# Performance work log

Measured on AMD Instinct MI355X. Metric: run time of the kernel, lower is better.

## Reference

```python
import jax, jax.numpy as jnp
import numpy as np

BSZ, SEQ, EMBED = 2, 4096, 1024
NUM_HEADS = 16
HEAD_DIM = EMBED // NUM_HEADS
WINDOW = 256  # attention_window[layer_id]


def setup_inputs() -> dict:
    key = jax.random.key(0)
    ks = jax.random.split(key, 7)
    s = 1.0 / np.sqrt(EMBED)
    return {
        "hidden_states": jax.random.normal(ks[0], (BSZ, SEQ, EMBED), jnp.float32),
        "Wq": jax.random.normal(ks[1], (EMBED, EMBED), jnp.float32) * s,
        "bq": jnp.zeros((EMBED,), jnp.float32),
        "Wk": jax.random.normal(ks[2], (EMBED, EMBED), jnp.float32) * s,
        "bk": jnp.zeros((EMBED,), jnp.float32),
        "Wv": jax.random.normal(ks[3], (EMBED, EMBED), jnp.float32) * s,
        "bv": jnp.zeros((EMBED,), jnp.float32),
    }


def _blocks3(x, nb, w):
    # x: [b, s + 2w, h, d] -> [b, nb, 3w, h, d]; block c sees key blocks c-1, c, c+1
    b = x.shape[0]
    xb = x.reshape(b, nb + 2, w, NUM_HEADS, HEAD_DIM)
    return jnp.concatenate([xb[:, i:i + nb] for i in range(3)], axis=2)


def reference(hidden_states, Wq, bq, Wk, bk, Wv, bv):
    b, s, e = hidden_states.shape
    w = WINDOW
    nb = s // w
    q = (hidden_states @ Wq + bq) * (1.0 / np.sqrt(HEAD_DIM))
    k = hidden_states @ Wk + bk
    v = hidden_states @ Wv + bv
    q = q.reshape(b, nb, w, NUM_HEADS, HEAD_DIM)
    k = k.reshape(b, s, NUM_HEADS, HEAD_DIM)
    v = v.reshape(b, s, NUM_HEADS, HEAD_DIM)
    pad = ((0, 0), (w, w), (0, 0), (0, 0))
    kb = _blocks3(jnp.pad(k, pad), nb, w)  # [b, nb, 3w, h, d]
    vb = _blocks3(jnp.pad(v, pad), nb, w)
    # banded scores: query x in block n attends keys at global pos n*w - w + y
    scores = jnp.einsum('bnxhd,bnyhd->bnhxy', q, kb)  # [b, nb, h, w, 3w]
    x_idx = jnp.arange(w)
    y_idx = jnp.arange(3 * w)
    band = jnp.abs(y_idx[None, :] - x_idx[:, None] - w) <= w  # [w, 3w]
    kpos = jnp.arange(nb)[:, None] * w - w + y_idx[None, :]   # [nb, 3w]
    inb = (kpos >= 0) & (kpos < s)
    mask = band[None, :, :] & inb[:, None, :]                 # [nb, w, 3w]
    scores = jnp.where(mask[None, :, None, :, :], scores, -jnp.inf)
    probs = jax.nn.softmax(scores.astype(jnp.float32), axis=-1).astype(v.dtype)
    attn = jnp.einsum('bnhxy,bnyhd->bnxhd', probs, vb)        # [b, nb, w, h, d]
    return attn.reshape(b, s, e)
```

## Files before the change

### kernel.cpp

```cpp
#include <hip/hip_runtime.h>
#include <stdint.h>

#define SEQ    4096
#define EMBED  1024
#define NHEAD  16
#define HDIM   64
#define WIN    256
#define BSZ    2
#define M_TOT  (BSZ * SEQ)
#define N_QKV  3072
#define N_QK   2048
#define K_DIM  1024
#define LOG2E  1.4426950408889634f

typedef __attribute__((ext_vector_type(8))) __bf16 bf16x8;
typedef __attribute__((ext_vector_type(4))) float  f32x4;

__device__ __forceinline__ unsigned short f2bf(float f) {
  union { float f; unsigned int u; } c; c.f = f;
  unsigned int u = c.u;
  unsigned int r = (u + 0x7FFFu + ((u >> 16) & 1u)) >> 16;
  return (unsigned short)r;
}

__device__ __forceinline__ unsigned int cvt_pk_bf16(float lo, float hi) {
  unsigned int r;
  asm("v_cvt_pk_bf16_f32 %0, %1, %2" : "=v"(r) : "v"(lo), "v"(hi));
  return r;
}

__device__ __forceinline__ void gl2lds16(const void* g, void* l) {
  __builtin_amdgcn_global_load_lds((const __attribute__((address_space(1))) void*)g,
                                   (__attribute__((address_space(3))) void*)l, 16, 0, 0);
}

__global__ __launch_bounds__(256) void cvt_h(const float* __restrict__ in,
                                             unsigned short* __restrict__ out) {
  int i = (blockIdx.x * 256 + threadIdx.x) * 4;
  float4 v = *(const float4*)(in + i);
  ushort4 o;
  o.x = f2bf(v.x); o.y = f2bf(v.y); o.z = f2bf(v.z); o.w = f2bf(v.w);
  *(ushort4*)(out + i) = o;
}

__global__ __launch_bounds__(256) void cvt_w(const float* __restrict__ Wq,
                                             const float* __restrict__ Wk,
                                             const float* __restrict__ Wv,
                                             unsigned short* __restrict__ Wt) {
  __shared__ float t[32][33];
  int z = blockIdx.z;
  const float* W = (z == 0) ? Wq : (z == 1) ? Wk : Wv;
  int kb = blockIdx.x * 32, nb = blockIdx.y * 32;
  int tx = threadIdx.x, ty = threadIdx.y;
  for (int it = 0; it < 4; ++it) {
    int k = kb + ty + it * 8;
    t[ty + it * 8][tx] = W[(size_t)k * 1024 + nb + tx];
  }
  __syncthreads();
  for (int it = 0; it < 4; ++it) {
    int n = nb + ty + it * 8;
    Wt[(size_t)(z * 1024 + n) * 1024 + kb + tx] = f2bf(t[tx][ty + it * 8]);
  }
}

__global__ __launch_bounds__(512, 2) void qkv_gemm(const unsigned short* __restrict__ A,
                                                   const unsigned short* __restrict__ Bt,
                                                   const float* __restrict__ bq,
                                                   const float* __restrict__ bk,
                                                   const float* __restrict__ bv,
                                                   unsigned short* __restrict__ C,
                                                   unsigned short* __restrict__ Vt) {
  __shared__ unsigned short As[2][256 * 64];
  __shared__ unsigned short Bs[2][256 * 64];
  int tid  = threadIdx.x;
  int lane = tid & 63, wave = tid >> 6;
  int ln   = lane & 15, quad = lane >> 4;
  int flat = blockIdx.y * 12 + blockIdx.x;
  int swz  = (flat & 7) * 48 + (flat >> 3);
  int m0 = (swz / 12) * 256, n0 = (swz % 12) * 256;
  int wy = wave >> 2, wx = wave & 3;
  f32x4 acc[8][4];
  for (int i = 0; i < 8; ++i)
    for (int j = 0; j < 4; ++j) acc[i][j] = (f32x4){0.f, 0.f, 0.f, 0.f};

#define STAGE(buf, k0)                                                          \
  do {                                                                          \
    for (int sweep = 0; sweep < 4; ++sweep) {                                   \
      int chunk = sweep * 512 + tid;                               \
      int row = chunk >> 3, c = chunk & 7;                                      \
      int cg = c ^ (row & 7);                                                   \
      gl2lds16(A + (size_t)(m0 + row) * K_DIM + (k0) + cg * 8,                  \
               &As[buf][chunk * 8]);                                            \
    }                                                                           \
    for (int sweep = 0; sweep < 4; ++sweep) {                                   \
      int chunk = sweep * 512 + tid;                                            \
      int row = chunk >> 3, c = chunk & 7;                                      \
      int cg = c ^ (row & 7);                                                   \
      gl2lds16(Bt + (size_t)(n0 + row) * K_DIM + (k0) + cg * 8,                 \
               &Bs[buf][chunk * 8]);                                            \
    }                                                                           \
  } while (0)

  STAGE(0, 0);
  __syncthreads();

  for (int t = 0; t < 16; ++t) {
    int cur = t & 1;
    if (t < 15) { STAGE(cur ^ 1, (t + 1) * 64); }
    const unsigned short* as = As[cur];
    const unsigned short* bs = Bs[cur];
    for (int ks2 = 0; ks2 < 2; ++ks2) {
      bf16x8 af[8], bfr[4];
      for (int i = 0; i < 8; ++i) {
        int row = wy * 128 + i * 16 + ln;
        int c = (ks2 * 4 + quad) ^ (row & 7);
        af[i] = *(const bf16x8*)&as[row * 64 + c * 8];
      }
      for (int j = 0; j < 4; ++j) {
        int row = wx * 64 + j * 16 + ln;
        int c = (ks2 * 4 + quad) ^ (row & 7);
        bfr[j] = *(const bf16x8*)&bs[row * 64 + c * 8];
      }
      __builtin_amdgcn_s_setprio(1);
      for (int i = 0; i < 8; ++i)
        for (int j = 0; j < 4; ++j)
          acc[i][j] = __builtin_amdgcn_mfma_f32_16x16x32_bf16(af[i], bfr[j], acc[i][j], 0, 0, 0);
      __builtin_amdgcn_s_setprio(0);
    }
    __syncthreads();
  }
#undef STAGE

  if (n0 < N_QK) {
    for (int j = 0; j < 4; ++j) {
      int n = n0 + wx * 64 + j * 16 + ln;
      float bias, scl;
      if (n < 1024) { bias = bq[n];        scl = 0.125f * LOG2E; }
      else          { bias = bk[n - 1024]; scl = 1.f; }
      for (int i = 0; i < 8; ++i) {
        int mb = m0 + wy * 128 + i * 16 + quad * 4;
        for (int r = 0; r < 4; ++r) {
          float v = (acc[i][j][r] + bias) * scl;
          C[(size_t)(mb + r) * N_QK + n] = f2bf(v);
        }
      }
    }
  } else {
    for (int j = 0; j < 4; ++j) {
      int n  = n0 + wx * 64 + j * 16 + ln;
      int hd = n - 2048;
      float bias = bv[hd];
      for (int i = 0; i < 8; ++i) {
        int mb  = m0 + wy * 128 + i * 16 + quad * 4;
        int bb  = mb >> 12;
        int pos = mb & (SEQ - 1);
        ushort4 pk;
        pk.x = f2bf(acc[i][j][0] + bias);
        pk.y = f2bf(acc[i][j][1] + bias);
        pk.z = f2bf(acc[i][j][2] + bias);
        pk.w = f2bf(acc[i][j][3] + bias);
        *(ushort4*)&Vt[((size_t)bb * (NHEAD * HDIM) + hd) * SEQ + pos] = pk;
      }
    }
  }
}

__global__ __launch_bounds__(256) void attn(const unsigned short* __restrict__ qk,
                                            const unsigned short* __restrict__ vtg,
                                            float* __restrict__ out) {
  __shared__ unsigned short Kl[64 * 72];
  __shared__ unsigned short Vl[64 * 72];
  int tid  = threadIdx.x;
  int lane = tid & 63, wave = tid >> 6;
  int ln   = lane & 15, quad = lane >> 4;
  int bx = blockIdx.x;
  int lx = ((bx & 7) << 3) | (bx >> 3);
  int q0 = lx * 64, head = blockIdx.y, b = blockIdx.z;
  size_t baseRow = (size_t)b * SEQ;
  const unsigned short* kptr = qk + 1024;
  const unsigned short* vrow = vtg + ((size_t)(b * NHEAD + head) * HDIM) * SEQ;

  int sy = tid >> 3, sc = tid & 7;
  const unsigned short* kbase = kptr + (baseRow + sy) * (size_t)N_QK + head * HDIM + sc * 8;
  const unsigned short* vbase = vrow + (size_t)sy * SEQ + sc * 8;

  bf16x8 qf[2];
  {
    size_t ro = (baseRow + q0 + wave * 16 + ln) * (size_t)N_QK + head * HDIM + quad * 8;
    qf[0] = *(const bf16x8*)&qk[ro];
    qf[1] = *(const bf16x8*)&qk[ro + 32];
  }

  float l_st = 0.f;
  f32x4 o_acc[4];
  for (int dt = 0; dt < 4; ++dt) o_acc[dt] = (f32x4){0.f, 0.f, 0.f, 0.f};

  int lo = (q0 >= 256) ? 0 : (256 - q0) / 64;
  int hi = (SEQ + 256 - q0) / 64; if (hi > 9) hi = 9;

  uint4 pk0, pk1, pv0, pv1;
#define PREFETCH(KT)                                                        \
  {                                                                         \
    pk0 = *(const uint4*)&kbase[(size_t)(KT) * N_QK];                       \
    pk1 = *(const uint4*)&kbase[(size_t)((KT) + 32) * N_QK];                \
    pv0 = *(const uint4*)&vbase[(KT)];                                      \
    pv1 = *(const uint4*)&vbase[(size_t)32 * SEQ + (KT)];                   \
  }

  PREFETCH(q0 - 256 + lo * 64);

  int srcA = ((lane & 16) << 1) | ln;
  int srcB = srcA + 16;
  bool hiQ = (lane & 32) != 0;

  for (int t = lo; t < hi; ++t) {
    int kt = q0 - 256 + t * 64;
    __syncthreads();
    *(uint4*)&Kl[sy * 72 + sc * 8]        = pk0;
    *(uint4*)&Kl[(sy + 32) * 72 + sc * 8] = pk1;
    *(uint4*)&Vl[sy * 72 + sc * 8]        = pv0;
    *(uint4*)&Vl[(sy + 32) * 72 + sc * 8] = pv1;
    __syncthreads();

    if (t + 1 < hi) { PREFETCH(kt + 64); }

    f32x4 s[4];
    __builtin_amdgcn_s_setprio(1);
    for (int nt = 0; nt < 4; ++nt) {
      bf16x8 kf0 = *(const bf16x8*)&Kl[(nt * 16 + ln) * 72 + quad * 8];
      bf16x8 kf1 = *(const bf16x8*)&Kl[(nt * 16 + ln) * 72 + 32 + quad * 8];
      f32x4 z = (f32x4){0.f, 0.f, 0.f, 0.f};
      z = __builtin_amdgcn_mfma_f32_16x16x32_bf16(kf0, qf[0], z, 0, 0, 0);
      z = __builtin_amdgcn_mfma_f32_16x16x32_bf16(kf1, qf[1], z, 0, 0, 0);
      s[nt] = z;
    }
    __builtin_amdgcn_s_setprio(0);

    if (t == 0 || t == 8) {
      int qq = q0 + wave * 16 + ln;
      for (int nt = 0; nt < 4; ++nt) {
        int kb = kt + nt * 16 + quad * 4 - qq;
        for (int r = 0; r < 4; ++r) {
          int dd = kb + r;
          if (dd < -WIN || dd > WIN) s[nt][r] = -INFINITY;
        }
      }
    }

    float rs = 0.f;
    for (int nt = 0; nt < 4; ++nt)
      for (int r = 0; r < 4; ++r) {
        float p = exp2f(s[nt][r]);
        s[nt][r] = p;
        rs += p;
      }
    l_st += rs;

    unsigned int p01[4], p23[4];
    for (int nt = 0; nt < 4; ++nt) {
      p01[nt] = cvt_pk_bf16(s[nt][0], s[nt][1]);
      p23[nt] = cvt_pk_bf16(s[nt][2], s[nt][3]);
    }

    for (int ks = 0; ks < 2; ++ks) {
      int ntA = 2 * ks, ntB = 2 * ks + 1;
      unsigned int a0 = (unsigned int)__shfl((int)p01[ntA], srcA);
      unsigned int a1 = (unsigned int)__shfl((int)p23[ntA], srcA);
      unsigned int a2 = (unsigned int)__shfl((int)p01[ntA], srcB);
      unsigned int a3 = (unsigned int)__shfl((int)p23[ntA], srcB);
      unsigned int b0 = (unsigned int)__shfl((int)p01[ntB], srcA);
      unsigned int b1 = (unsigned int)__shfl((int)p23[ntB], srcA);
      unsigned int b2 = (unsigned int)__shfl((int)p01[ntB], srcB);
      unsigned int b3 = (unsigned int)__shfl((int)p23[ntB], srcB);
      union { uint4 u; bf16x8 v; } pf;
      pf.u.x = hiQ ? b0 : a0;
      pf.u.y = hiQ ? b1 : a1;
      pf.u.z = hiQ ? b2 : a2;
      pf.u.w = hiQ ? b3 : a3;
      __builtin_amdgcn_s_setprio(1);
      for (int dt = 0; dt < 4; ++dt) {
        bf16x8 vf = *(const bf16x8*)&Vl[(dt * 16 + ln) * 72 + ks * 32 + quad * 8];
        o_acc[dt] = __builtin_amdgcn_mfma_f32_16x16x32_bf16(vf, pf.v, o_acc[dt], 0, 0, 0);
      }
      __builtin_amdgcn_s_setprio(0);
    }
  }

  float l = l_st;
  l += __shfl_xor(l, 16);
  l += __shfl_xor(l, 32);
  float inv = 1.0f / l;
  int qpos = q0 + wave * 16 + ln;
  float* ob = out + (baseRow + qpos) * (size_t)EMBED + head * HDIM + quad * 4;
  for (int dt = 0; dt < 4; ++dt) {
    float4 v;
    v.x = o_acc[dt][0] * inv;
    v.y = o_acc[dt][1] * inv;
    v.z = o_acc[dt][2] * inv;
    v.w = o_acc[dt][3] * inv;
    *(float4*)(ob + dt * 16) = v;
  }
#undef PREFETCH
}

extern "C" void kernel_launch(void* const* d_in, const int* in_sizes, int n_in,
                              void* d_out, int out_size, void* d_ws, size_t ws_size,
                              hipStream_t stream) {
  const float* h  = (const float*)d_in[0];
  const float* Wq = (const float*)d_in[1];
  const float* bq = (const float*)d_in[2];
  const float* Wk = (const float*)d_in[3];
  const float* bk = (const float*)d_in[4];
  const float* Wv = (const float*)d_in[5];
  const float* bv = (const float*)d_in[6];
  float* out = (float*)d_out;

  unsigned short* h_bf  = (unsigned short*)d_ws;
  unsigned short* wt_bf = h_bf + (size_t)M_TOT * K_DIM;
  unsigned short* qk    = wt_bf + (size_t)N_QKV * K_DIM;
  unsigned short* vtg   = qk + (size_t)M_TOT * N_QK;

  cvt_h<<<(M_TOT * K_DIM) / 1024, 256, 0, stream>>>(h, h_bf);
  cvt_w<<<dim3(32, 32, 3), dim3(32, 8), 0, stream>>>(Wq, Wk, Wv, wt_bf);
  qkv_gemm<<<dim3(12, 32), 512, 0, stream>>>(h_bf, wt_bf, bq, bk, bv, qk, vtg);
  attn<<<dim3(SEQ / 64, NHEAD, BSZ), 256, 0, stream>>>(qk, vtg, out);
}
```

Baseline: 220.7 us.

## Split QKV GEMM tile into quadrant-staged pipeline with interleaved async loads

Restructures the QKV GEMM main loop into four quadrant MFMA phases. The next K-tile's A and B halves are issued as async global-to-LDS loads between those phases, gated by explicit vmcnt waits and raw s_barrier instead of one bulk stage followed by __syncthreads. Fragment loads are reordered so the A and B quarters are reused across phases, and the loops are fully unrolled. The aim is to hide global memory latency under the MFMA work with finer-grained overlap. The cost is more barriers per iteration and fragile hand-managed waitcnt/buffer reuse ordering.

Result: faster. 214.5 us (-2.8%).

```diff
diff --git a/kernel.cpp b/kernel.cpp
--- a/kernel.cpp
+++ b/kernel.cpp
@@ -80,65 +80,158 @@
   int m0 = (swz / 12) * 256, n0 = (swz % 12) * 256;
   int wy = wave >> 2, wx = wave & 3;
   f32x4 acc[8][4];
+#pragma unroll
   for (int i = 0; i < 8; ++i)
+#pragma unroll
     for (int j = 0; j < 4; ++j) acc[i][j] = (f32x4){0.f, 0.f, 0.f, 0.f};
 
-#define STAGE(buf, k0)                                                          \
-  do {                                                                          \
-    for (int sweep = 0; sweep < 4; ++sweep) {                                   \
-      int chunk = sweep * 512 + tid;                               \
-      int row = chunk >> 3, c = chunk & 7;                                      \
-      int cg = c ^ (row & 7);                                                   \
-      gl2lds16(A + (size_t)(m0 + row) * K_DIM + (k0) + cg * 8,                  \
-               &As[buf][chunk * 8]);                                            \
-    }                                                                           \
-    for (int sweep = 0; sweep < 4; ++sweep) {                                   \
-      int chunk = sweep * 512 + tid;                                            \
-      int row = chunk >> 3, c = chunk & 7;                                      \
-      int cg = c ^ (row & 7);                                                   \
-      gl2lds16(Bt + (size_t)(n0 + row) * K_DIM + (k0) + cg * 8,                 \
-               &Bs[buf][chunk * 8]);                                            \
-    }                                                                           \
+  int c8 = tid & 7;
+  int aR[2][2], bR[2][2];
+#pragma unroll
+  for (int s = 0; s < 2; ++s) {
+    int rir = s * 64 + (tid >> 3);
+    int la = (rir & 63) | ((rir & 64) << 1);
+    int lb = (rir & 31) | ((rir >> 5) << 6);
+    aR[0][s] = la;  aR[1][s] = la + 64;
+    bR[0][s] = lb;  bR[1][s] = lb + 32;
+  }
+
+#define STG_A(buf, half, kt)                                                     \
+  do {                                                                           \
+    _Pragma("unroll")                                                            \
+    for (int s = 0; s < 2; ++s) {                                                \
+      int lr = aR[half][s]; int cg = c8 ^ (lr & 7);                              \
+      gl2lds16(A + (size_t)(m0 + lr) * K_DIM + (kt) * 64 + cg * 8,               \
+               &As[buf][lr * 64 + c8 * 8]);                                      \
+    }                                                                            \
   } while (0)
-
-  STAGE(0, 0);
-  __syncthreads();
-
+#define STG_B(buf, half, kt)                                                     \
+  do {                                                                           \
+    _Pragma("unroll")                                                            \
+    for (int s = 0; s < 2; ++s) {                                                \
+      int lr = bR[half][s]; int cg = c8 ^ (lr & 7);                              \
+      gl2lds16(Bt + (size_t)(n0 + lr) * K_DIM + (kt) * 64 + cg * 8,              \
+               &Bs[buf][lr * 64 + c8 * 8]);                                      \
+    }                                                                            \
+  } while (0)
+
+  STG_A(0, 0, 0); STG_B(0, 0, 0); STG_B(0, 1, 0); STG_A(0, 1, 0);
+  STG_A(1, 0, 1); STG_B(1, 0, 1); STG_B(1, 1, 1);
+  asm volatile("s_waitcnt vmcnt(6)" ::: "memory");
+  __builtin_amdgcn_s_barrier();
+
+  bf16x8 af[4][2], bv0[2][2], bv1[2][2];
+  int aBase = wy * 128, bBase = wx * 64;
+
+#pragma unroll 1
   for (int t = 0; t < 16; ++t) {
     int cur = t & 1;
-    if (t < 15) { STAGE(cur ^ 1, (t + 1) * 64); }
     const unsigned short* as = As[cur];
     const unsigned short* bs = Bs[cur];
-    for (int ks2 = 0; ks2 < 2; ++ks2) {
-      bf16x8 af[8], bfr[4];
-      for (int i = 0; i < 8; ++i) {
-        int row = wy * 128 + i * 16 + ln;
-        int c = (ks2 * 4 + quad) ^ (row & 7);
-        af[i] = *(const bf16x8*)&as[row * 64 + c * 8];
-      }
-      for (int j = 0; j < 4; ++j) {
-        int row = wx * 64 + j * 16 + ln;
-        int c = (ks2 * 4 + quad) ^ (row & 7);
-        bfr[j] = *(const bf16x8*)&bs[row * 64 + c * 8];
-      }
-      __builtin_amdgcn_s_setprio(1);
-      for (int i = 0; i < 8; ++i)
-        for (int j = 0; j < 4; ++j)
-          acc[i][j] = __builtin_amdgcn_mfma_f32_16x16x32_bf16(af[i], bfr[j], acc[i][j], 0, 0, 0);
-      __builtin_amdgcn_s_setprio(0);
-    }
-    __syncthreads();
-  }
-#undef STAGE
+
+#pragma unroll
+    for (int i2 = 0; i2 < 4; ++i2) {
+      int row = aBase + i2 * 16 + ln;
+#pragma unroll
+      for (int ks = 0; ks < 2; ++ks) {
+        int c = (ks * 4 + quad) ^ (row & 7);
+        af[i2][ks] = *(const bf16x8*)&as[row * 64 + c * 8];
+      }
+    }
+#pragma unroll
+    for (int j2 = 0; j2 < 2; ++j2) {
+      int row = bBase + j2 * 16 + ln;
+#pragma unroll
+      for (int ks = 0; ks < 2; ++ks) {
+        int c = (ks * 4 + quad) ^ (row & 7);
+        bv0[j2][ks] = *(const bf16x8*)&bs[row * 64 + c * 8];
+      }
+    }
+    if (t < 15) STG_A(cur ^ 1, 1, t + 1);
+    __builtin_amdgcn_s_barrier();
+    __builtin_amdgcn_s_setprio(1);
+#pragma unroll
+    for (int ks = 0; ks < 2; ++ks)
+#pragma unroll
+      for (int i2 = 0; i2 < 4; ++i2)
+#pragma unroll
+        for (int j2 = 0; j2 < 2; ++j2)
+          acc[i2][j2] = __builtin_amdgcn_mfma_f32_16x16x32_bf16(af[i2][ks], bv0[j2][ks], acc[i2][j2], 0, 0, 0);
+    __builtin_amdgcn_s_setprio(0);
+    __builtin_amdgcn_s_barrier();
+
+#pragma unroll
+    for (int j2 = 0; j2 < 2; ++j2) {
+      int row = bBase + 32 + j2 * 16 + ln;
+#pragma unroll
+      for (int ks = 0; ks < 2; ++ks) {
+        int c = (ks * 4 + quad) ^ (row & 7);
+        bv1[j2][ks] = *(const bf16x8*)&bs[row * 64 + c * 8];
+      }
+    }
+    if (t < 14) STG_A(cur, 0, t + 2);
+    __builtin_amdgcn_s_barrier();
+    __builtin_amdgcn_s_setprio(1);
+#pragma unroll
+    for (int ks = 0; ks < 2; ++ks)
+#pragma unroll
+      for (int i2 = 0; i2 < 4; ++i2)
+#pragma unroll
+        for (int j2 = 0; j2 < 2; ++j2)
+          acc[i2][2 + j2] = __builtin_amdgcn_mfma_f32_16x16x32_bf16(af[i2][ks], bv1[j2][ks], acc[i2][2 + j2], 0, 0, 0);
+    __builtin_amdgcn_s_setprio(0);
+    __builtin_amdgcn_s_barrier();
+
+#pragma unroll
+    for (int i2 = 0; i2 < 4; ++i2) {
+      int row = aBase + 64 + i2 * 16 + ln;
+#pragma unroll
+      for (int ks = 0; ks < 2; ++ks) {
+        int c = (ks * 4 + quad) ^ (row & 7);
+        af[i2][ks] = *(const bf16x8*)&as[row * 64 + c * 8];
+      }
+    }
+    if (t < 14) STG_B(cur, 0, t + 2);
+    __builtin_amdgcn_s_barrier();
+    __builtin_amdgcn_s_setprio(1);
+#pragma unroll
+    for (int ks = 0; ks < 2; ++ks)
+#pragma unroll
+      for (int i2 = 0; i2 < 4; ++i2)
+#pragma unroll
+        for (int j2 = 0; j2 < 2; ++j2)
+          acc[4 + i2][j2] = __builtin_amdgcn_mfma_f32_16x16x32_bf16(af[i2][ks], bv0[j2][ks], acc[4 + i2][j2], 0, 0, 0);
+    __builtin_amdgcn_s_setprio(0);
+    __builtin_amdgcn_s_barrier();
+
+    if (t < 14) STG_B(cur, 1, t + 2);
+    __builtin_amdgcn_s_barrier();
+    __builtin_amdgcn_s_setprio(1);
+#pragma unroll
+    for (int ks = 0; ks < 2; ++ks)
+#pragma unroll
+      for (int i2 = 0; i2 < 4; ++i2)
+#pragma unroll
+        for (int j2 = 0; j2 < 2; ++j2)
+          acc[4 + i2][2 + j2] = __builtin_amdgcn_mfma_f32_16x16x32_bf16(af[i2][ks], bv1[j2][ks], acc[4 + i2][2 + j2], 0, 0, 0);
+    __builtin_amdgcn_s_setprio(0);
+    asm volatile("s_waitcnt vmcnt(6)" ::: "memory");
+    __builtin_amdgcn_s_barrier();
+  }
+#undef STG_A
+#undef STG_B
 
   if (n0 < N_QK) {
+#pragma unroll
     for (int j = 0; j < 4; ++j) {
       int n = n0 + wx * 64 + j * 16 + ln;
       float bias, scl;
       if (n < 1024) { bias = bq[n];        scl = 0.125f * LOG2E; }
       else          { bias = bk[n - 1024]; scl = 1.f; }
+#pragma unroll
       for (int i = 0; i < 8; ++i) {
         int mb = m0 + wy * 128 + i * 16 + quad * 4;
+#pragma unroll
         for (int r = 0; r < 4; ++r) {
           float v = (acc[i][j][r] + bias) * scl;
           C[(size_t)(mb + r) * N_QK + n] = f2bf(v);
@@ -146,10 +239,12 @@
       }
     }
   } else {
+#pragma unroll
     for (int j = 0; j < 4; ++j) {
       int n  = n0 + wx * 64 + j * 16 + ln;
       int hd = n - 2048;
       float bias = bv[hd];
+#pragma unroll
       for (int i = 0; i < 8; ++i) {
         int mb  = m0 + wy * 128 + i * 16 + quad * 4;
         int bb  = mb >> 12;
```
